# Performance work log

Hardware: AMD Instinct MI355X
Metric: run time of the kernel (lower is better)

Reference implementation:

```python
import jax, jax.numpy as jnp
import numpy as np

N = 50000          # nodes
E = 800000         # edges per metapath
M = 3              # metapaths
IN_DIM = 256
H = 8              # heads
D = 32             # out_dim per head
HID = 128          # semantic attention hidden
NEG_SLOPE = 0.2    # DGL GATConv default leaky_relu slope


def setup_inputs() -> dict:
    key = jax.random.key(0)
    ks = jax.random.split(key, 10)
    h = jax.random.normal(ks[0], (N, IN_DIM), dtype=jnp.float32)
    src = jax.random.randint(ks[1], (M, E), 0, N, dtype=jnp.int32)
    dst = jax.random.randint(ks[2], (M, E), 0, N, dtype=jnp.int32)
    s = 1.0 / np.sqrt(IN_DIM)
    fc_w = jax.random.normal(ks[3], (M, IN_DIM, H * D), dtype=jnp.float32) * s
    attn_l = jax.random.normal(ks[4], (M, H, D), dtype=jnp.float32) * 0.1
    attn_r = jax.random.normal(ks[5], (M, H, D), dtype=jnp.float32) * 0.1
    bias = jnp.zeros((M, H * D), dtype=jnp.float32)
    sem_w1 = jax.random.normal(ks[6], (H * D, HID), dtype=jnp.float32) * (1.0 / np.sqrt(H * D))
    sem_b1 = jnp.zeros((HID,), dtype=jnp.float32)
    sem_w2 = jax.random.normal(ks[7], (HID, 1), dtype=jnp.float32) * (1.0 / np.sqrt(HID))
    return {"h": h, "src": src, "dst": dst, "fc_w": fc_w, "attn_l": attn_l,
            "attn_r": attn_r, "bias": bias, "sem_w1": sem_w1, "sem_b1": sem_b1,
            "sem_w2": sem_w2}


def _gat(h, src, dst, fc_w, attn_l, attn_r, bias):
    # DGL GATConv (eval mode, dropout=0), activation=elu.
    feat = (h @ fc_w).reshape(N, H, D)                       # [N,H,D]
    el = jnp.sum(feat * attn_l, axis=-1)                     # [N,H]
    er = jnp.sum(feat * attn_r, axis=-1)                     # [N,H]
    e = jax.nn.leaky_relu(el[src] + er[dst], NEG_SLOPE)      # [E,H]
    # edge softmax over incoming edges of each dst node
    emax = jax.ops.segment_max(e, dst, num_segments=N)       # [N,H]
    emax = jnp.where(jnp.isfinite(emax), emax, 0.0)
    ee = jnp.exp(e - emax[dst])                              # [E,H]
    esum = jax.ops.segment_sum(ee, dst, num_segments=N)      # [N,H]
    alpha = ee / jnp.maximum(esum[dst], 1e-38)               # [E,H]
    msg = feat[src] * alpha[:, :, None]                      # [E,H,D]
    rst = jax.ops.segment_sum(msg, dst, num_segments=N)      # [N,H,D]
    rst = rst + bias.reshape(1, H, D)
    return jax.nn.elu(rst).reshape(N, H * D)                 # flatten heads


def reference(h, src, dst, fc_w, attn_l, attn_r, bias, sem_w1, sem_b1, sem_w2):
    gat_all = jax.vmap(_gat, in_axes=(None, 0, 0, 0, 0, 0, 0))
    z_m = gat_all(h, src, dst, fc_w, attn_l, attn_r, bias)   # [M,N,F]
    z_m = jnp.transpose(z_m, (1, 0, 2))                      # [N,M,F]
    # semantic attention
    w = jnp.tanh(z_m @ sem_w1 + sem_b1) @ sem_w2             # [N,M,1]
    w = w.mean(axis=0)                                       # [M,1]
    a_w = jax.nn.softmax(w, axis=0)                          # [M,1]
    z = jnp.sum(z_m * a_w[None, :, :], axis=1)               # [N,F]
    return z
```

## Files before the change

### kernel.cpp

```cpp
#include <hip/hip_runtime.h>
#include <math.h>

#define NN   50000
#define EE   800000
#define MM   3
#define KDIM 256
#define FF   256
#define HH   8
#define DD   32
#define HID  128
#define SLOPE 0.2f
#define BK   32
#define PAD  40
#define CAP  80

typedef unsigned short u16;
typedef unsigned int   u32;
typedef __attribute__((ext_vector_type(8))) short short8;
typedef __attribute__((ext_vector_type(4))) float floatx4;

__device__ __forceinline__ float eluf(float x) { return x > 0.f ? x : expm1f(x); }

__device__ __forceinline__ float b2f(u16 u) {
    union { u32 i; float f; } v; v.i = ((u32)u) << 16; return v.f;
}
__device__ __forceinline__ u16 f2b(float f) {
    union { float f; u32 i; } v; v.f = f;
    u32 lsb = (v.i >> 16) & 1u;
    v.i += 0x7fffu + lsb;
    return (u16)(v.i >> 16);
}
__device__ __forceinline__ u32 pack2(float lo, float hi) {
    return (u32)f2b(lo) | ((u32)f2b(hi) << 16);
}

__global__ __launch_bounds__(256) void k_cast_w(
    const float* __restrict__ fcw, u16* __restrict__ fcwt)
{
    int k = blockIdx.x, m = blockIdx.y, n = threadIdx.x;
    float v = fcw[((size_t)m * KDIM + k) * FF + n];
    fcwt[((size_t)m * FF + n) * KDIM + k] = f2b(v);
}

__global__ __launch_bounds__(128) void k_cast_w1(
    const float* __restrict__ w1, u16* __restrict__ w1t)
{
    int k = blockIdx.x, n = threadIdx.x;
    w1t[(size_t)n * KDIM + k] = f2b(w1[(size_t)k * HID + n]);
}

__global__ __launch_bounds__(256) void k_scatter_fixed(
    const int* __restrict__ src, const int* __restrict__ dst,
    int* __restrict__ cnt, u16* __restrict__ srt)
{
    long long eg = (long long)blockIdx.x * 256 + threadIdx.x;
    if (eg < (long long)MM * EE) {
        int m = (int)(eg / EE);
        int d = dst[eg];
        int slot = atomicAdd(&cnt[(size_t)m * NN + d], 1);
        if (slot < CAP) srt[(size_t)(m * CAP + slot) * NN + d] = (u16)src[eg];
    }
}

__global__ __launch_bounds__(256) void k_feat_all(
    const float* __restrict__ hmat,
    const u16*   __restrict__ fcwt,
    const float* __restrict__ al,
    const float* __restrict__ ar,
    u16*   __restrict__ featb,
    float* __restrict__ el,
    float* __restrict__ er)
{
    __shared__ u16 As[128 * PAD];
    __shared__ u16 Bs[128 * PAD];

    const int n0 = blockIdx.x * 128;
    const int cy = blockIdx.y;
    const int m  = blockIdx.z;
    const int c_base = cy * 128;
    const int t = threadIdx.x;
    const int wave = t >> 6, lane = t & 63;
    const int wr = wave >> 1, wc = wave & 1;
    const int quad = lane >> 4, l15 = lane & 15;

    const u16* fcwt_m = fcwt + (size_t)m * FF * KDIM;
    const float* al_m = al + (size_t)m * HH * DD;
    const float* ar_m = ar + (size_t)m * HH * DD;

    floatx4 acc[4][4] = {};

    for (int k0 = 0; k0 < KDIM; k0 += BK) {
        __syncthreads();
        #pragma unroll
        for (int i = 0; i < 2; ++i) {
            int flat = i * 256 + t;
            int r = flat >> 2, seg = flat & 3;
            int n = n0 + r;
            uint4 u = make_uint4(0u, 0u, 0u, 0u);
            if (n < NN) {
                const float* p = hmat + (size_t)n * KDIM + k0 + seg * 8;
                float4 v0 = *(const float4*)p;
                float4 v1 = *(const float4*)(p + 4);
                u.x = pack2(v0.x, v0.y); u.y = pack2(v0.z, v0.w);
                u.z = pack2(v1.x, v1.y); u.w = pack2(v1.z, v1.w);
            }
            *(uint4*)(&As[r * PAD + seg * 8]) = u;
        }
        #pragma unroll
        for (int i = 0; i < 2; ++i) {
            int flat = i * 256 + t;
            int r = flat >> 2, seg = flat & 3;
            uint4 u = *(const uint4*)(fcwt_m + (size_t)(c_base + r) * KDIM + k0 + seg * 8);
            *(uint4*)(&Bs[r * PAD + seg * 8]) = u;
        }
        __syncthreads();

        short8 afr[4], bfr[4];
        #pragma unroll
        for (int ti = 0; ti < 4; ++ti)
            afr[ti] = *(const short8*)(&As[(wr * 64 + ti * 16 + l15) * PAD + quad * 8]);
        #pragma unroll
        for (int tj = 0; tj < 4; ++tj)
            bfr[tj] = *(const short8*)(&Bs[(wc * 64 + tj * 16 + l15) * PAD + quad * 8]);
        #pragma unroll
        for (int ti = 0; ti < 4; ++ti)
            #pragma unroll
            for (int tj = 0; tj < 4; ++tj)
                acc[ti][tj] = __builtin_amdgcn_mfma_f32_16x16x32_bf16(
                    afr[ti], bfr[tj], acc[ti][tj], 0, 0, 0);
    }

    float alv[4], arv[4];
    #pragma unroll
    for (int tj = 0; tj < 4; ++tj) {
        int h = cy * 4 + wc * 2 + (tj >> 1);
        int dcol = (tj & 1) * 16 + l15;
        alv[tj] = al_m[h * DD + dcol];
        arv[tj] = ar_m[h * DD + dcol];
    }
    const int h0 = cy * 4 + wc * 2, h1 = h0 + 1;

    #pragma unroll
    for (int ti = 0; ti < 4; ++ti) {
        #pragma unroll
        for (int reg = 0; reg < 4; ++reg) {
            int n = n0 + wr * 64 + ti * 16 + quad * 4 + reg;
            bool ok = n < NN;
            if (ok) {
                #pragma unroll
                for (int tj = 0; tj < 4; ++tj) {
                    int c = c_base + wc * 64 + tj * 16 + l15;
                    featb[((size_t)m * NN + n) * FF + c] = f2b(acc[ti][tj][reg]);
                }
            }
            float pl0 = acc[ti][0][reg] * alv[0] + acc[ti][1][reg] * alv[1];
            float pl1 = acc[ti][2][reg] * alv[2] + acc[ti][3][reg] * alv[3];
            float pr0 = acc[ti][0][reg] * arv[0] + acc[ti][1][reg] * arv[1];
            float pr1 = acc[ti][2][reg] * arv[2] + acc[ti][3][reg] * arv[3];
            #pragma unroll
            for (int s = 1; s < 16; s <<= 1) {
                pl0 += __shfl_xor(pl0, s); pl1 += __shfl_xor(pl1, s);
                pr0 += __shfl_xor(pr0, s); pr1 += __shfl_xor(pr1, s);
            }
            if (l15 == 0 && ok) {
                el[((size_t)m * NN + n) * HH + h0] = pl0;
                el[((size_t)m * NN + n) * HH + h1] = pl1;
                er[((size_t)m * NN + n) * HH + h0] = pr0;
                er[((size_t)m * NN + n) * HH + h1] = pr1;
            }
        }
    }
}

__global__ __launch_bounds__(256) void k_aggr_all(
    const int* __restrict__ cnt,
    const u16* __restrict__ srt,
    const float* __restrict__ el,
    const float* __restrict__ er,
    const u16* __restrict__ featb,
    const float* __restrict__ bias,
    u16* __restrict__ z)
{
    __shared__ float alpha_s[4][CAP * HH];
    __shared__ int   src_s[4][CAP];

    const int m = blockIdx.y;
    const int wave = threadIdx.x >> 6, lane = threadIdx.x & 63;
    const int d = blockIdx.x * 4 + wave;

    const int deg = min(cnt[(size_t)m * NN + d], CAP);
    const float* el_m = el + (size_t)m * NN * HH;
    const u16* feat_m = featb + (size_t)m * NN * FF;

    if (lane < deg)
        src_s[wave][lane] = (int)srt[(size_t)(m * CAP + lane) * NN + d];
    if (64 + lane < deg)
        src_s[wave][64 + lane] = (int)srt[(size_t)(m * CAP + 64 + lane) * NN + d];

    const int hA = lane & 7;
    const float er_d = er[((size_t)m * NN + d) * HH + hA];
    float esum_r = 0.f;
    const int nIter = (deg + 7) >> 3;
    for (int i = 0; i < nIter; ++i) {
        int j = i * 8 + (lane >> 3);
        float e = 0.f;
        if (j < deg) {
            int s = src_s[wave][j];
            float x = el_m[(size_t)s * HH + hA] + er_d;
            x = x >= 0.f ? x : SLOPE * x;
            x = fminf(x, 60.f);
            e = expf(x);
            alpha_s[wave][j * HH + hA] = e;
        }
        float g = e;
        g += __shfl_xor(g, 8); g += __shfl_xor(g, 16); g += __shfl_xor(g, 32);
        esum_r += g;
    }
    float inv_r = 1.f / fmaxf(esum_r, 1e-38f);

    const float inv_g = __shfl(inv_r, lane >> 3);
    float4 acc = make_float4(0.f, 0.f, 0.f, 0.f);
    const int hB = lane >> 3;
    for (int j = 0; j < deg; ++j) {
        int s = src_s[wave][j];
        float a = alpha_s[wave][j * HH + hB] * inv_g;
        uint2 f = *(const uint2*)(feat_m + (size_t)s * FF + lane * 4);
        acc.x += a * b2f((u16)(f.x & 0xffff));
        acc.y += a * b2f((u16)(f.x >> 16));
        acc.z += a * b2f((u16)(f.y & 0xffff));
        acc.w += a * b2f((u16)(f.y >> 16));
    }
    float4 b = *(const float4*)(bias + (size_t)m * FF + lane * 4);
    uint2 o;
    o.x = pack2(eluf(acc.x + b.x), eluf(acc.y + b.y));
    o.y = pack2(eluf(acc.z + b.z), eluf(acc.w + b.w));
    *(uint2*)(z + ((size_t)m * NN + d) * FF + lane * 4) = o;
}

__global__ __launch_bounds__(256) void k_sem_all(
    const u16* __restrict__ z,
    const u16* __restrict__ w1t,
    const float* __restrict__ b1,
    const float* __restrict__ w2,
    float* __restrict__ wsum)
{
    __shared__ u16 As[128 * PAD];
    __shared__ u16 Bs[128 * PAD];

    const int n0 = blockIdx.x * 128;
    const int m  = blockIdx.y;
    const int t = threadIdx.x;
    const int wave = t >> 6, lane = t & 63;
    const int wr = wave >> 1, wc = wave & 1;
    const int quad = lane >> 4, l15 = lane & 15;

    const u16* z_m = z + (size_t)m * NN * FF;

    floatx4 acc[4][4] = {};

    for (int k0 = 0; k0 < KDIM; k0 += BK) {
        __syncthreads();
        #pragma unroll
        for (int i = 0; i < 2; ++i) {
            int flat = i * 256 + t;
            int r = flat >> 2, seg = flat & 3;
            int n = n0 + r;
            uint4 u = make_uint4(0u, 0u, 0u, 0u);
            if (n < NN) u = *(const uint4*)(z_m + (size_t)n * FF + k0 + seg * 8);
            *(uint4*)(&As[r * PAD + seg * 8]) = u;
        }
        #pragma unroll
        for (int i = 0; i < 2; ++i) {
            int flat = i * 256 + t;
            int r = flat >> 2, seg = flat & 3;
            if (r < HID) {
                uint4 u = *(const uint4*)(w1t + (size_t)r * KDIM + k0 + seg * 8);
                *(uint4*)(&Bs[r * PAD + seg * 8]) = u;
            }
        }
        __syncthreads();

        short8 afr[4], bfr[4];
        #pragma unroll
        for (int ti = 0; ti < 4; ++ti)
            afr[ti] = *(const short8*)(&As[(wr * 64 + ti * 16 + l15) * PAD + quad * 8]);
        #pragma unroll
        for (int tj = 0; tj < 4; ++tj)
            bfr[tj] = *(const short8*)(&Bs[(wc * 64 + tj * 16 + l15) * PAD + quad * 8]);
        #pragma unroll
        for (int ti = 0; ti < 4; ++ti)
            #pragma unroll
            for (int tj = 0; tj < 4; ++tj)
                acc[ti][tj] = __builtin_amdgcn_mfma_f32_16x16x32_bf16(
                    afr[ti], bfr[tj], acc[ti][tj], 0, 0, 0);
    }

    float b1v[4], w2v[4];
    #pragma unroll
    for (int tj = 0; tj < 4; ++tj) {
        int c = wc * 64 + tj * 16 + l15;
        b1v[tj] = b1[c];
        w2v[tj] = w2[c];
    }
    float local = 0.f;
    #pragma unroll
    for (int ti = 0; ti < 4; ++ti) {
        #pragma unroll
        for (int reg = 0; reg < 4; ++reg) {
            int n = n0 + wr * 64 + ti * 16 + quad * 4 + reg;
            if (n < NN) {
                #pragma unroll
                for (int tj = 0; tj < 4; ++tj)
                    local += tanhf(acc[ti][tj][reg] + b1v[tj]) * w2v[tj];
            }
        }
    }
    #pragma unroll
    for (int s = 1; s < 64; s <<= 1) local += __shfl_xor(local, s);
    if (lane == 0) atomicAdd(&wsum[m], local);
}

__global__ __launch_bounds__(256) void k_combine(
    const u16* __restrict__ z, const float* __restrict__ wsum,
    float* __restrict__ out)
{
    float s0 = wsum[0] / (float)NN, s1 = wsum[1] / (float)NN, s2 = wsum[2] / (float)NN;
    float mx = fmaxf(s0, fmaxf(s1, s2));
    float e0 = expf(s0 - mx), e1 = expf(s1 - mx), e2 = expf(s2 - mx);
    float inv = 1.f / (e0 + e1 + e2);
    float aw[3] = { e0 * inv, e1 * inv, e2 * inv };

    long long idx = (long long)blockIdx.x * 256 + threadIdx.x;
    if (idx >= (long long)NN * 64) return;
    int n = (int)(idx >> 6), c = (int)(idx & 63) * 4;
    float4 o = make_float4(0.f, 0.f, 0.f, 0.f);
    #pragma unroll
    for (int m = 0; m < MM; ++m) {
        uint2 zu = *(const uint2*)(z + ((size_t)m * NN + n) * FF + c);
        float a = aw[m];
        o.x += a * b2f((u16)(zu.x & 0xffff));
        o.y += a * b2f((u16)(zu.x >> 16));
        o.z += a * b2f((u16)(zu.y & 0xffff));
        o.w += a * b2f((u16)(zu.y >> 16));
    }
    *(float4*)(out + (size_t)n * FF + c) = o;
}

extern "C" void kernel_launch(void* const* d_in, const int* in_sizes, int n_in,
                              void* d_out, int out_size, void* d_ws, size_t ws_size,
                              hipStream_t stream)
{
    const float* hmat = (const float*)d_in[0];
    const int*   src  = (const int*)d_in[1];
    const int*   dst  = (const int*)d_in[2];
    const float* fcw  = (const float*)d_in[3];
    const float* al   = (const float*)d_in[4];
    const float* ar   = (const float*)d_in[5];
    const float* bias = (const float*)d_in[6];
    const float* w1   = (const float*)d_in[7];
    const float* b1   = (const float*)d_in[8];
    const float* w2   = (const float*)d_in[9];
    float* out = (float*)d_out;

    char* ws = (char*)d_ws;
    size_t off = 0;
    auto alloc = [&](size_t nbytes) {
        void* p = (void*)(ws + off);
        off = (off + nbytes + 255) & ~(size_t)255;
        return p;
    };
    float* el   = (float*)alloc((size_t)MM * NN * HH * 4);
    float* er   = (float*)alloc((size_t)MM * NN * HH * 4);
    float* wsum = (float*)alloc(256);
    int*   cnt  = (int*)alloc((size_t)MM * NN * 4);
    u16*   srt  = (u16*)alloc((size_t)MM * CAP * NN * 2);
    u16*   fcwt = (u16*)alloc((size_t)MM * KDIM * FF * 2);
    u16*   w1t  = (u16*)alloc((size_t)HID * KDIM * 2);
    u16*   featb= (u16*)alloc((size_t)MM * NN * FF * 2);
    u16*   z    = (u16*)alloc((size_t)MM * NN * FF * 2);

    hipMemsetAsync(wsum, 0, 256, stream);
    hipMemsetAsync(cnt, 0, (size_t)MM * NN * 4, stream);

    k_cast_w<<<dim3(KDIM, MM), 256, 0, stream>>>(fcw, fcwt);
    k_cast_w1<<<KDIM, 128, 0, stream>>>(w1, w1t);

    long long ne = (long long)MM * EE;
    k_scatter_fixed<<<(int)((ne + 255) / 256), 256, 0, stream>>>(src, dst, cnt, srt);

    k_feat_all<<<dim3((NN + 127) / 128, 2, MM), 256, 0, stream>>>(
        hmat, fcwt, al, ar, featb, el, er);
    k_aggr_all<<<dim3(NN / 4, MM), 256, 0, stream>>>(cnt, srt, el, er, featb, bias, z);
    k_sem_all<<<dim3((NN + 127) / 128, MM), 256, 0, stream>>>(z, w1t, b1, w2, wsum);
    k_combine<<<(NN * 64 + 255) / 256, 256, 0, stream>>>(z, wsum, out);
}
```

Measured before the change: 613.8 us.

## Pre-cast h to bf16, process two dst nodes per wave with 16-byte gathers

```diff
diff --git a/kernel.cpp b/kernel.cpp
--- a/kernel.cpp
+++ b/kernel.cpp
@@ -21,8 +21,11 @@
 
 __device__ __forceinline__ float eluf(float x) { return x > 0.f ? x : expm1f(x); }
 
-__device__ __forceinline__ float b2f(u16 u) {
-    union { u32 i; float f; } v; v.i = ((u32)u) << 16; return v.f;
+__device__ __forceinline__ float b2f_lo(u32 u) {
+    union { u32 i; float f; } v; v.i = u << 16; return v.f;
+}
+__device__ __forceinline__ float b2f_hi(u32 u) {
+    union { u32 i; float f; } v; v.i = u & 0xffff0000u; return v.f;
 }
 __device__ __forceinline__ u16 f2b(float f) {
     union { float f; u32 i; } v; v.f = f;
@@ -32,6 +35,19 @@
 }
 __device__ __forceinline__ u32 pack2(float lo, float hi) {
     return (u32)f2b(lo) | ((u32)f2b(hi) << 16);
+}
+
+__global__ __launch_bounds__(256) void k_cast_h(
+    const float* __restrict__ hmat, u16* __restrict__ hb)
+{
+    long long i = ((long long)blockIdx.x * 256 + threadIdx.x) * 8;
+    if (i >= (long long)NN * KDIM) return;
+    float4 v0 = *(const float4*)(hmat + i);
+    float4 v1 = *(const float4*)(hmat + i + 4);
+    uint4 u;
+    u.x = pack2(v0.x, v0.y); u.y = pack2(v0.z, v0.w);
+    u.z = pack2(v1.x, v1.y); u.w = pack2(v1.z, v1.w);
+    *(uint4*)(hb + i) = u;
 }
 
 __global__ __launch_bounds__(256) void k_cast_w(
@@ -63,7 +79,7 @@
 }
 
 __global__ __launch_bounds__(256) void k_feat_all(
-    const float* __restrict__ hmat,
+    const u16*   __restrict__ hb,
     const u16*   __restrict__ fcwt,
     const float* __restrict__ al,
     const float* __restrict__ ar,
@@ -97,13 +113,7 @@
             int r = flat >> 2, seg = flat & 3;
             int n = n0 + r;
             uint4 u = make_uint4(0u, 0u, 0u, 0u);
-            if (n < NN) {
-                const float* p = hmat + (size_t)n * KDIM + k0 + seg * 8;
-                float4 v0 = *(const float4*)p;
-                float4 v1 = *(const float4*)(p + 4);
-                u.x = pack2(v0.x, v0.y); u.y = pack2(v0.z, v0.w);
-                u.z = pack2(v1.x, v1.y); u.w = pack2(v1.z, v1.w);
-            }
+            if (n < NN) u = *(const uint4*)(hb + (size_t)n * KDIM + k0 + seg * 8);
             *(uint4*)(&As[r * PAD + seg * 8]) = u;
         }
         #pragma unroll
@@ -181,60 +191,70 @@
     const float* __restrict__ bias,
     u16* __restrict__ z)
 {
-    __shared__ float alpha_s[4][CAP * HH];
-    __shared__ int   src_s[4][CAP];
+    __shared__ float alpha_s[4][2][CAP][HH];
+    __shared__ int   srcoff[4][2][CAP];
 
     const int m = blockIdx.y;
     const int wave = threadIdx.x >> 6, lane = threadIdx.x & 63;
-    const int d = blockIdx.x * 4 + wave;
+    const int half = lane >> 5, L = lane & 31;
+    const int d = blockIdx.x * 8 + wave * 2 + half;
 
     const int deg = min(cnt[(size_t)m * NN + d], CAP);
     const float* el_m = el + (size_t)m * NN * HH;
     const u16* feat_m = featb + (size_t)m * NN * FF;
 
-    if (lane < deg)
-        src_s[wave][lane] = (int)srt[(size_t)(m * CAP + lane) * NN + d];
-    if (64 + lane < deg)
-        src_s[wave][64 + lane] = (int)srt[(size_t)(m * CAP + 64 + lane) * NN + d];
-
-    const int hA = lane & 7;
+    #pragma unroll
+    for (int i = 0; i < 3; ++i) {
+        int slot = L + i * 32;
+        if (slot < deg)
+            srcoff[wave][half][slot] =
+                (int)srt[(size_t)(m * CAP + slot) * NN + d] * FF;
+    }
+
+    const int hA = L & 7;
     const float er_d = er[((size_t)m * NN + d) * HH + hA];
     float esum_r = 0.f;
-    const int nIter = (deg + 7) >> 3;
+    const int nIter = (deg + 3) >> 2;
     for (int i = 0; i < nIter; ++i) {
-        int j = i * 8 + (lane >> 3);
+        int j = i * 4 + (L >> 3);
         float e = 0.f;
         if (j < deg) {
-            int s = src_s[wave][j];
-            float x = el_m[(size_t)s * HH + hA] + er_d;
+            int so = srcoff[wave][half][j];
+            float x = el_m[(size_t)(so >> 5) + hA] + er_d;
             x = x >= 0.f ? x : SLOPE * x;
             x = fminf(x, 60.f);
             e = expf(x);
-            alpha_s[wave][j * HH + hA] = e;
+            alpha_s[wave][half][j][hA] = e;
         }
         float g = e;
-        g += __shfl_xor(g, 8); g += __shfl_xor(g, 16); g += __shfl_xor(g, 32);
+        g += __shfl_xor(g, 8); g += __shfl_xor(g, 16);
         esum_r += g;
     }
     float inv_r = 1.f / fmaxf(esum_r, 1e-38f);
 
-    const float inv_g = __shfl(inv_r, lane >> 3);
-    float4 acc = make_float4(0.f, 0.f, 0.f, 0.f);
-    const int hB = lane >> 3;
+    const float inv_g = __shfl(inv_r, (lane & 32) | (L >> 2));
+    const int hB = L >> 2;
+    float acc[8] = {0.f, 0.f, 0.f, 0.f, 0.f, 0.f, 0.f, 0.f};
     for (int j = 0; j < deg; ++j) {
-        int s = src_s[wave][j];
-        float a = alpha_s[wave][j * HH + hB] * inv_g;
-        uint2 f = *(const uint2*)(feat_m + (size_t)s * FF + lane * 4);
-        acc.x += a * b2f((u16)(f.x & 0xffff));
-        acc.y += a * b2f((u16)(f.x >> 16));
-        acc.z += a * b2f((u16)(f.y & 0xffff));
-        acc.w += a * b2f((u16)(f.y >> 16));
-    }
-    float4 b = *(const float4*)(bias + (size_t)m * FF + lane * 4);
-    uint2 o;
-    o.x = pack2(eluf(acc.x + b.x), eluf(acc.y + b.y));
-    o.y = pack2(eluf(acc.z + b.z), eluf(acc.w + b.w));
-    *(uint2*)(z + ((size_t)m * NN + d) * FF + lane * 4) = o;
+        int so = srcoff[wave][half][j];
+        float a = alpha_s[wave][half][j][hB];
+        uint4 f = *(const uint4*)(feat_m + (size_t)so + L * 8);
+        acc[0] += a * b2f_lo(f.x); acc[1] += a * b2f_hi(f.x);
+        acc[2] += a * b2f_lo(f.y); acc[3] += a * b2f_hi(f.y);
+        acc[4] += a * b2f_lo(f.z); acc[5] += a * b2f_hi(f.z);
+        acc[6] += a * b2f_lo(f.w); acc[7] += a * b2f_hi(f.w);
+    }
+    #pragma unroll
+    for (int k = 0; k < 8; ++k) acc[k] *= inv_g;
+
+    const float4 b0 = *(const float4*)(bias + (size_t)m * FF + L * 8);
+    const float4 b1 = *(const float4*)(bias + (size_t)m * FF + L * 8 + 4);
+    uint4 o;
+    o.x = pack2(eluf(acc[0] + b0.x), eluf(acc[1] + b0.y));
+    o.y = pack2(eluf(acc[2] + b0.z), eluf(acc[3] + b0.w));
+    o.z = pack2(eluf(acc[4] + b1.x), eluf(acc[5] + b1.y));
+    o.w = pack2(eluf(acc[6] + b1.z), eluf(acc[7] + b1.w));
+    *(uint4*)(z + ((size_t)m * NN + d) * FF + L * 8) = o;
 }
 
 __global__ __launch_bounds__(256) void k_sem_all(
@@ -331,19 +351,21 @@
     float aw[3] = { e0 * inv, e1 * inv, e2 * inv };
 
     long long idx = (long long)blockIdx.x * 256 + threadIdx.x;
-    if (idx >= (long long)NN * 64) return;
-    int n = (int)(idx >> 6), c = (int)(idx & 63) * 4;
-    float4 o = make_float4(0.f, 0.f, 0.f, 0.f);
+    if (idx >= (long long)NN * 32) return;
+    int n = (int)(idx >> 5), c = (int)(idx & 31) * 8;
+    float acc[8] = {0.f, 0.f, 0.f, 0.f, 0.f, 0.f, 0.f, 0.f};
     #pragma unroll
     for (int m = 0; m < MM; ++m) {
-        uint2 zu = *(const uint2*)(z + ((size_t)m * NN + n) * FF + c);
+        uint4 f = *(const uint4*)(z + ((size_t)m * NN + n) * FF + c);
         float a = aw[m];
-        o.x += a * b2f((u16)(zu.x & 0xffff));
-        o.y += a * b2f((u16)(zu.x >> 16));
-        o.z += a * b2f((u16)(zu.y & 0xffff));
-        o.w += a * b2f((u16)(zu.y >> 16));
-    }
-    *(float4*)(out + (size_t)n * FF + c) = o;
+        acc[0] += a * b2f_lo(f.x); acc[1] += a * b2f_hi(f.x);
+        acc[2] += a * b2f_lo(f.y); acc[3] += a * b2f_hi(f.y);
+        acc[4] += a * b2f_lo(f.z); acc[5] += a * b2f_hi(f.z);
+        acc[6] += a * b2f_lo(f.w); acc[7] += a * b2f_hi(f.w);
+    }
+    float* op = out + (size_t)n * FF + c;
+    *(float4*)op       = make_float4(acc[0], acc[1], acc[2], acc[3]);
+    *(float4*)(op + 4) = make_float4(acc[4], acc[5], acc[6], acc[7]);
 }
 
 extern "C" void kernel_launch(void* const* d_in, const int* in_sizes, int n_in,
@@ -376,12 +398,14 @@
     u16*   srt  = (u16*)alloc((size_t)MM * CAP * NN * 2);
     u16*   fcwt = (u16*)alloc((size_t)MM * KDIM * FF * 2);
     u16*   w1t  = (u16*)alloc((size_t)HID * KDIM * 2);
+    u16*   hb   = (u16*)alloc((size_t)NN * KDIM * 2);
     u16*   featb= (u16*)alloc((size_t)MM * NN * FF * 2);
     u16*   z    = (u16*)alloc((size_t)MM * NN * FF * 2);
 
     hipMemsetAsync(wsum, 0, 256, stream);
     hipMemsetAsync(cnt, 0, (size_t)MM * NN * 4, stream);
 
+    k_cast_h<<<(int)(((size_t)NN * KDIM / 8 + 255) / 256), 256, 0, stream>>>(hmat, hb);
     k_cast_w<<<dim3(KDIM, MM), 256, 0, stream>>>(fcw, fcwt);
     k_cast_w1<<<KDIM, 128, 0, stream>>>(w1, w1t);
 
@@ -389,8 +413,8 @@
     k_scatter_fixed<<<(int)((ne + 255) / 256), 256, 0, stream>>>(src, dst, cnt, srt);
 
     k_feat_all<<<dim3((NN + 127) / 128, 2, MM), 256, 0, stream>>>(
-        hmat, fcwt, al, ar, featb, el, er);
-    k_aggr_all<<<dim3(NN / 4, MM), 256, 0, stream>>>(cnt, srt, el, er, featb, bias, z);
+        hb, fcwt, al, ar, featb, el, er);
+    k_aggr_all<<<dim3(NN / 8, MM), 256, 0, stream>>>(cnt, srt, el, er, featb, bias, z);
     k_sem_all<<<dim3((NN + 127) / 128, MM), 256, 0, stream>>>(z, w1t, b1, w2, wsum);
-    k_combine<<<(NN * 64 + 255) / 256, 256, 0, stream>>>(z, wsum, out);
-}
+    k_combine<<<(int)(((size_t)NN * 32 + 255) / 256), 256, 0, stream>>>(z, wsum, out);
+}
```

Measured after the change: 601.2 us. 2.1% less time.
